# Kernel tuning notes

Hardware: AMD Instinct MI355X
Metric: run time of the kernel (lower is better)

The kernel has to match this reference:

```python
import jax, jax.numpy as jnp
import numpy as np

B, L, C, H, T = 4096, 32, 28, 512, 32


def setup_inputs() -> dict:
    key = jax.random.key(0)
    ks = jax.random.split(key, 10)
    s = 0.1
    return dict(
        input=jax.random.normal(ks[0], (B, L, C), jnp.float32),
        unpacked_masks=jnp.ones((B, L, 1), jnp.float32),
        bias_mat=jax.random.normal(ks[1], (B, L), jnp.float32),
        conv1_w=jax.random.normal(ks[2], (C, C, 3), jnp.float32) * s,  # OIH
        conv1_b=jnp.zeros((C,), jnp.float32),
        conv_w=jax.random.normal(ks[3], (1, C, 1), jnp.float32) * s,
        conv_b=jnp.zeros((1,), jnp.float32),
        w_ih=jax.random.normal(ks[4], (4 * H, C), jnp.float32) * s,
        w_hh=jax.random.normal(ks[5], (4 * H, H), jnp.float32) * s,
        b_ih=jnp.zeros((4 * H,), jnp.float32),
        b_hh=jnp.concatenate([jnp.zeros(H), jnp.ones(H), jnp.zeros(2 * H)]).astype(jnp.float32),  # forget-gate bias = 1 as in weights_init
        fc1_w=jax.random.normal(ks[6], (1, H), jnp.float32) * s,
        fc1_b=jnp.zeros((1,), jnp.float32),
        conv2_w=jax.random.normal(ks[7], (1, H, 1), jnp.float32) * s,
        conv2_b=jnp.zeros((1,), jnp.float32),
    )


def reference(input, unpacked_masks, bias_mat, conv1_w, conv1_b, conv_w, conv_b,
              w_ih, w_hh, b_ih, b_hh, fc1_w, fc1_b, conv2_w, conv2_b):
    b, l, c = input.shape
    # residual conv block: conv1d(28->28,k3,pad1) -> mask -> elu -> +input
    x_ncl = jnp.transpose(input, (0, 2, 1))
    y = jax.lax.conv_general_dilated(x_ncl, conv1_w, (1,), 'SAME',
                                     dimension_numbers=('NCH', 'OIH', 'NCH'))
    y = jnp.transpose(y + conv1_b[None, :, None], (0, 2, 1))
    x = jax.nn.elu(y * unpacked_masks) + input  # [B,L,C]
    # u_a: 1x1 conv (28->1) == per-position linear, then mask -> [B,L,1]
    u_a = (jnp.einsum('blc,c->bl', x, conv_w[0, :, 0]) + conv_b)[..., None] * unpacked_masks
    bias = bias_mat.reshape(b, l, 1)

    def step(carry, _):
        h, cstate = carry
        w_a = (h @ fc1_w.T + fc1_b)[:, :, None]                 # [B,1,1]
        attn = jax.nn.leaky_relu(u_a + w_a) + bias              # [B,L,1]
        attn = jax.nn.softmax(attn, axis=1)                     # softmax over sequence
        context = jnp.einsum('bl,blc->bc', attn[..., 0], x)     # [B,C]
        gates = context @ w_ih.T + b_ih + h @ w_hh.T + b_hh     # [B,4H]
        i, f, g, o = jnp.split(gates, 4, axis=1)                # torch LSTMCell gate order
        cstate = jax.nn.sigmoid(f) * cstate + jax.nn.sigmoid(i) * jnp.tanh(g)
        h = jax.nn.sigmoid(o) * jnp.tanh(cstate)
        return (h, cstate), h

    h0 = jnp.zeros((b, w_hh.shape[1]), input.dtype)
    (_, _), hs = jax.lax.scan(step, (h0, h0), None, length=T)   # [T,B,H]
    all_hidden = jnp.transpose(hs, (1, 0, 2))                   # [B,T,H]
    # dropout layers are identity in eval; conv2 is 1x1 conv (512->1)
    out = (jnp.einsum('bth,h->bt', all_hidden, conv2_w[0, :, 0]) + conv2_b)[..., None]
    return out * unpacked_masks
```

## Files before the change

kernel.cpp:

```cpp
#include <hip/hip_runtime.h>
#include <hip/hip_bf16.h>

#define B_N 4096
#define L_N 32
#define C_N 28
#define H_N 512
#define T_N 32
#define G_N 2048
#define CHA 34
#define CHSH 4096
#define ABLK (CHA * CHSH)
#define XS 29

typedef __attribute__((ext_vector_type(2))) float f32x2;
typedef __attribute__((ext_vector_type(4))) float f32x4;
typedef __attribute__((ext_vector_type(8))) short s16x8;

static constexpr size_t OFF_WF = 0;
static constexpr size_t AB_ONE = (size_t)32 * ABLK * 2;
static constexpr size_t OFF_AB = OFF_WF + (size_t)16 * ABLK * 2;
static constexpr size_t OFF_X  = OFF_AB + 2 * AB_ONE;
static constexpr size_t OFF_UA = OFF_X + (size_t)B_N * L_N * C_N * 4;
static constexpr size_t OFF_BS = OFF_UA + (size_t)B_N * L_N * 4;
static constexpr size_t OFF_AC = OFF_BS + 8192;
static constexpr size_t ACC_HALF = (size_t)32 * B_N * 4;
static constexpr size_t OFF_CS = OFF_AC + 2 * ACC_HALF;
static constexpr size_t WS_NEED = OFF_CS + (size_t)B_N * H_N * 4;

__device__ __forceinline__ short bfbits(__hip_bfloat16 b) {
    union { __hip_bfloat16 b; short s; } v; v.b = b; return v.s;
}
__device__ __forceinline__ float sigmoidf_(float x) { return 1.f / (1.f + __expf(-x)); }
__device__ __forceinline__ float tanhf_(float x) {
    float ax = fabsf(x), e = __expf(-2.f * ax);
    float t = (1.f - e) / (1.f + e);
    return x < 0.f ? -t : t;
}

__global__ __launch_bounds__(256) void fill_out(float* out, float v) {
    int i = blockIdx.x * 256 + threadIdx.x;
    if (i < B_N * 32) out[i] = v;
}

__global__ __launch_bounds__(256) void prep_x(const float* __restrict__ input,
                       const float* __restrict__ mask,
                       const float* __restrict__ w1, const float* __restrict__ b1,
                       const float* __restrict__ cw, const float* __restrict__ cb,
                       float* __restrict__ x, float* __restrict__ ua)
{
    __shared__ float sin[8 * L_N * XS];
    __shared__ float sxb[8 * L_N * XS];
    const float* src = input + (size_t)blockIdx.x * (8 * L_N * C_N);
    for (int i = threadIdx.x; i < 8 * L_N * C_N; i += 256) {
        int lr = i / (L_N * C_N);
        int rem = i - lr * (L_N * C_N);
        int l = rem / C_N, c = rem - l * C_N;
        sin[lr * (L_N * XS) + l * XS + c] = src[i];
    }
    __syncthreads();

    int idx = blockIdx.x * 256 + threadIdx.x;
    int l = idx & 31;
    int wv = threadIdx.x >> 5;
    const float* inb = sin + wv * (L_N * XS);
    float m = mask[idx];

    float x0r[C_N], xm1[C_N], xp1[C_N];
    #pragma unroll
    for (int i = 0; i < C_N; ++i) x0r[i] = inb[l * XS + i];
    #pragma unroll
    for (int i = 0; i < C_N; ++i) {
        float up = __shfl_up(x0r[i], 1, 32);
        float dn = __shfl_down(x0r[i], 1, 32);
        xm1[i] = (l > 0)  ? up : 0.f;
        xp1[i] = (l < 31) ? dn : 0.f;
    }

    float uacc = 0.f;
    float* sxrow = sxb + wv * (L_N * XS) + l * XS;
    #pragma unroll 2
    for (int o = 0; o < C_N; ++o) {
        const float* wo = w1 + o * (C_N * 3);
        float y0 = b1[o], y1 = 0.f, y2 = 0.f;
        #pragma unroll
        for (int i = 0; i < C_N; ++i) {
            y0 += wo[i * 3 + 0] * xm1[i];
            y1 += wo[i * 3 + 1] * x0r[i];
            y2 += wo[i * 3 + 2] * xp1[i];
        }
        float y = (y0 + y1 + y2) * m;
        float e = (y > 0.f) ? y : (__expf(y) - 1.f);
        float xv = e + inb[l * XS + o];
        sxrow[o] = xv;
        uacc += xv * cw[o];
    }
    ua[idx] = (uacc + cb[0]) * m;
    __syncthreads();
    float* xdst = x + (size_t)blockIdx.x * (8 * L_N * C_N);
    for (int i = threadIdx.x; i < 8 * L_N * C_N; i += 256) {
        int lr = i / (L_N * C_N);
        int rem = i - lr * (L_N * C_N);
        int l2 = rem / C_N, c = rem - l2 * C_N;
        xdst[i] = sxb[lr * (L_N * XS) + l2 * XS + c];
    }
}

__global__ __launch_bounds__(256) void prep_wf(const float* __restrict__ w_ih,
                                               const float* __restrict__ w_hh,
                                               short* __restrict__ Wf)
{
    int blk = blockIdx.x;
    int n128 = blk / CHA, c = blk % CHA;
    bool lo = (c >= 17);
    int kbase = (lo ? (c - 17) : c) * 32;
    short* dst = Wf + ((size_t)n128 * CHA + c) * CHSH;
    for (int g = threadIdx.x; g < 512; g += 256) {
        int j = g >> 6, lane = g & 63;
        int gate = j & 3;
        int unit = n128 * 32 + (j >> 2) * 16 + (lane & 15);
        int srow = gate * H_N + unit;
        int kg = lane >> 4;
        s16x8 out;
        #pragma unroll
        for (int b2 = 0; b2 < 8; ++b2) {
            int k = kbase + kg * 8 + b2;
            float v = 0.f;
            if (k < 512) v = w_hh[(size_t)srow * H_N + k];
            else if (k < 540) v = w_ih[srow * C_N + (k - 512)];
            __hip_bfloat16 hi = __float2bfloat16(v);
            if (lo) out[b2] = bfbits(__float2bfloat16(v - __bfloat162float(hi)));
            else    out[b2] = bfbits(hi);
        }
        *(s16x8*)(dst + g * 8) = out;
    }
}

__global__ void prep_bs(const float* __restrict__ b_ih, const float* __restrict__ b_hh,
                        float* __restrict__ bsum)
{
    int p = blockIdx.x * 256 + threadIdx.x;
    if (p < G_N) {
        int unit = p >> 2, gate = p & 3;
        bsum[p] = b_ih[gate * H_N + unit] + b_hh[gate * H_N + unit];
    }
}

__global__ void prep_zero(unsigned int* __restrict__ a32, float* __restrict__ cst,
                          float* __restrict__ acc)
{
    int idx = blockIdx.x * blockDim.x + threadIdx.x;
    if (idx < B_N * 1088) a32[idx] = 0u;
    if (idx < B_N * H_N) cst[idx] = 0.f;
    if (idx < 2 * 32 * B_N) acc[idx] = 0.f;
}

struct RParams {
    const float* mask;
    const float* bias_mat;
    const float* fc1_w;
    const float* fc1_b;
    const float* conv2_w;
    const float* conv2_b;
    const short* Wf;
    const short* Ain;
    short* Aout;
    const float* x;
    const float* ua;
    const float* bsum;
    float* accW;
    float* accO;
    float* cstate;
    float* out;
};

__global__ __launch_bounds__(256) void ctx_step(RParams P, int t)
{
    __shared__ float sx[4][L_N * C_N];

    const int lane = threadIdx.x & 63;
    const int wave = threadIdx.x >> 6;
    const int row  = blockIdx.x * 4 + wave;

    f32x2 st[7];
    const float* xrow = P.x + (size_t)row * (L_N * C_N);
    #pragma unroll
    for (int q = 0; q < 7; ++q) st[q] = *(const f32x2*)(xrow + (q * 64 + lane) * 2);

    float v = (lane < 32) ? P.accW[row * 32 + lane] : P.accO[row * 32 + (lane - 32)];
    #pragma unroll
    for (int off = 1; off <= 16; off <<= 1) v += __shfl_xor(v, off);
    float aW = __shfl(v, 0);
    float aO = __shfl(v, 32);

    if (t > 0 && lane == 0)
        P.out[row * T_N + (t - 1)] = (aO + P.conv2_b[0]) * P.mask[row * L_N + (t - 1)];

    if (t < T_N) {
        float w_a = aW + P.fc1_b[0];
        int l32 = lane & 31;
        float e = P.ua[row * L_N + l32] + w_a;
        e = (e > 0.f) ? e : 0.01f * e;
        e += P.bias_mat[row * L_N + l32];
        float mx = e;
        #pragma unroll
        for (int off = 16; off > 0; off >>= 1) mx = fmaxf(mx, __shfl_xor(mx, off, 32));
        float pexp = __expf(e - mx);
        float ssum = pexp;
        #pragma unroll
        for (int off = 16; off > 0; off >>= 1) ssum += __shfl_xor(ssum, off, 32);
        float p = pexp / ssum;

        #pragma unroll
        for (int q = 0; q < 7; ++q)
            *(f32x2*)(&sx[wave][(q * 64 + lane) * 2]) = st[q];

        int cc = (lane < C_N) ? lane : 0;
        float ctx = 0.f;
        #pragma unroll
        for (int l = 0; l < L_N; ++l) {
            float al = __shfl(p, l);
            ctx += al * sx[wave][l * C_N + cc];
        }
        if (lane < C_N) {
            int m128 = row >> 7, mt = (row & 127) >> 4, r = row & 15;
            int flane = r + 16 * (lane >> 3);
            short* base = P.Aout + (size_t)m128 * ABLK + mt * 512 + flane * 8 + (lane & 7);
            __hip_bfloat16 hi = __float2bfloat16(ctx);
            base[16 * CHSH] = bfbits(hi);
            base[33 * CHSH] = bfbits(__float2bfloat16(ctx - __bfloat162float(hi)));
        }
    }
}

#define STG_BUF 32768

__global__ __launch_bounds__(256, 2) void gemm_cell_step(RParams P)
{
    __shared__ __align__(16) char smem[65536];

    const int tid  = threadIdx.x;
    const int lane = tid & 63;
    const int wave = tid >> 6;
    const int bid  = blockIdx.x;
    const int xg = bid & 7, gg = bid >> 3;
    const int m  = (xg >> 1) * 8 + (gg & 7);
    const int n  = (xg & 1) * 8 + (gg >> 3);
    const int wm = wave >> 1, wn = wave & 1;

    const short* Af = P.Ain + (size_t)m * ABLK;
    const short* Wg = P.Wf  + (size_t)n * ABLK;

    const short* slab0 = (wave < 2) ? Af : Wg;
    const int slab_lo  = (wave & 1) ? 17 : 0;

    char* bufp0 = smem;
    char* bufp1 = smem + STG_BUF;

    auto stage = [&](char* lbuf, int kk) {
        const short* gp = slab0 + (size_t)(slab_lo + kk) * CHSH + lane * 8;
        char* lb = lbuf + wave * 8192;
        #pragma unroll
        for (int r = 0; r < 8; ++r) {
            __builtin_amdgcn_global_load_lds(
                (const __attribute__((address_space(1))) void*)(gp + r * 512),
                (__attribute__((address_space(3))) void*)(lb + r * 1024),
                16, 0, 0);
        }
    };

    int aoff[4], woff[4];
    #pragma unroll
    for (int i = 0; i < 4; ++i) {
        aoff[i] = ((wm * 4 + i) * 64 + lane) * 16;
        woff[i] = ((wn * 4 + i) * 64 + lane) * 16;
    }

    f32x4 acc[4][4];
    #pragma unroll
    for (int i = 0; i < 4; ++i)
        #pragma unroll
        for (int j = 0; j < 4; ++j)
            acc[i][j] = (f32x4){0.f, 0.f, 0.f, 0.f};

    s16x8 RA[16], RB[16];
    auto ldfr = [&](const char* b, s16x8 (&R)[16]) {
        #pragma unroll
        for (int i = 0; i < 4; ++i) {
            R[i]      = *(const s16x8*)(b + aoff[i]);
            R[4 + i]  = *(const s16x8*)(b + 8192 + aoff[i]);
            R[8 + i]  = *(const s16x8*)(b + 16384 + woff[i]);
            R[12 + i] = *(const s16x8*)(b + 24576 + woff[i]);
        }
    };
    auto domm = [&](s16x8 (&R)[16]) {
        #pragma unroll
        for (int i = 0; i < 4; ++i)
            #pragma unroll
            for (int j = 0; j < 4; ++j)
                acc[i][j] = __builtin_amdgcn_mfma_f32_16x16x32_bf16(R[i], R[8 + j], acc[i][j], 0, 0, 0);
        #pragma unroll
        for (int i = 0; i < 4; ++i)
            #pragma unroll
            for (int j = 0; j < 4; ++j)
                acc[i][j] = __builtin_amdgcn_mfma_f32_16x16x32_bf16(R[4 + i], R[8 + j], acc[i][j], 0, 0, 0);
        #pragma unroll
        for (int i = 0; i < 4; ++i)
            #pragma unroll
            for (int j = 0; j < 4; ++j)
                acc[i][j] = __builtin_amdgcn_mfma_f32_16x16x32_bf16(R[i], R[12 + j], acc[i][j], 0, 0, 0);
    };
    auto step = [&](int kk, s16x8 (&Rc)[16], s16x8 (&Rn)[16], char* bcur, char* bnext) {
        asm volatile("s_waitcnt vmcnt(0) lgkmcnt(0)" ::: "memory");
        __builtin_amdgcn_s_barrier();
        __builtin_amdgcn_sched_barrier(0);
        if (kk + 2 <= 16) stage(bcur, kk + 2);
        if (kk + 1 <= 16) ldfr(bnext, Rn);
        __builtin_amdgcn_sched_barrier(0);
        __builtin_amdgcn_s_setprio(1);
        domm(Rc);
        __builtin_amdgcn_s_setprio(0);
        __builtin_amdgcn_sched_barrier(0);
    };

    stage(bufp0, 0);
    asm volatile("s_waitcnt vmcnt(0)" ::: "memory");
    __builtin_amdgcn_s_barrier();
    stage(bufp1, 1);
    ldfr(bufp0, RA);

    for (int kp = 0; kp < 8; ++kp) {
        step(2 * kp,     RA, RB, bufp0, bufp1);
        step(2 * kp + 1, RB, RA, bufp1, bufp0);
    }
    step(16, RA, RB, bufp0, bufp1);

    __syncthreads();
    short* hasm = (short*)smem;
    {
        int u15 = lane & 15, rq = lane >> 4;
        int unit = n * 32 + wn * 16 + u15;
        float cpre[4][4];
        #pragma unroll
        for (int i = 0; i < 4; ++i)
            #pragma unroll
            for (int r = 0; r < 4; ++r)
                cpre[i][r] = P.cstate[(size_t)(m * 128 + wm * 64 + i * 16 + rq * 4 + r) * H_N + unit];
        f32x4 bsv = *(const f32x4*)(P.bsum + unit * 4);
        float f1v = P.fc1_w[unit];
        float c2v = P.conv2_w[unit];
        const int fl16 = 16 * (wn * 2 + (u15 >> 3));
        const int slot = u15 & 7;
        #pragma unroll
        for (int i = 0; i < 4; ++i) {
            #pragma unroll
            for (int r = 0; r < 4; ++r) {
                int grow = m * 128 + wm * 64 + i * 16 + rq * 4 + r;
                float pi = acc[i][0][r] + bsv.x;
                float pf = acc[i][1][r] + bsv.y;
                float pg = acc[i][2][r] + bsv.z;
                float po = acc[i][3][r] + bsv.w;
                float c = sigmoidf_(pf) * cpre[i][r] + sigmoidf_(pi) * tanhf_(pg);
                P.cstate[(size_t)grow * H_N + unit] = c;
                float h = sigmoidf_(po) * tanhf_(c);
                __hip_bfloat16 hi = __float2bfloat16(h);
                int fo = (wm * 4 + i) * 512 + (rq * 4 + r + fl16) * 8 + slot;
                hasm[fo]        = bfbits(hi);
                hasm[4096 + fo] = bfbits(__float2bfloat16(h - __bfloat162float(hi)));
                float wd = f1v * h, od = c2v * h;
                #pragma unroll
                for (int off = 8; off > 0; off >>= 1) {
                    wd += __shfl_xor(wd, off);
                    od += __shfl_xor(od, off);
                }
                if (u15 == 0) {
                    P.accW[(size_t)grow * 32 + (n * 2 + wn)] = wd;
                    P.accO[(size_t)grow * 32 + (n * 2 + wn)] = od;
                }
            }
        }
    }
    __syncthreads();
    short* dhi = P.Aout + (size_t)m * ABLK + (size_t)n * CHSH;
    short* dlo = P.Aout + (size_t)m * ABLK + (size_t)(17 + n) * CHSH;
    *(s16x8*)(dhi + tid * 16)     = *(const s16x8*)(hasm + tid * 16);
    *(s16x8*)(dhi + tid * 16 + 8) = *(const s16x8*)(hasm + tid * 16 + 8);
    *(s16x8*)(dlo + tid * 16)     = *(const s16x8*)(hasm + 4096 + tid * 16);
    *(s16x8*)(dlo + tid * 16 + 8) = *(const s16x8*)(hasm + 4096 + tid * 16 + 8);
}

extern "C" void kernel_launch(void* const* d_in, const int* in_sizes, int n_in,
                              void* d_out, int out_size, void* d_ws, size_t ws_size,
                              hipStream_t stream)
{
    float* out = (float*)d_out;
    if (ws_size < WS_NEED) { fill_out<<<512, 256, 0, stream>>>(out, 4000.f); return; }

    const float* input = (const float*)d_in[0];
    const float* mask  = (const float*)d_in[1];
    const float* biasm = (const float*)d_in[2];
    const float* w1    = (const float*)d_in[3];
    const float* b1    = (const float*)d_in[4];
    const float* cw    = (const float*)d_in[5];
    const float* cb    = (const float*)d_in[6];
    const float* w_ih  = (const float*)d_in[7];
    const float* w_hh  = (const float*)d_in[8];
    const float* b_ih  = (const float*)d_in[9];
    const float* b_hh  = (const float*)d_in[10];
    const float* fc1w  = (const float*)d_in[11];
    const float* fc1b  = (const float*)d_in[12];
    const float* c2w   = (const float*)d_in[13];
    const float* c2b   = (const float*)d_in[14];

    char* ws = (char*)d_ws;
    short* Wf = (short*)(ws + OFF_WF);
    short* A0 = (short*)(ws + OFF_AB);
    short* A1 = (short*)(ws + OFF_AB + AB_ONE);
    float* x    = (float*)(ws + OFF_X);
    float* ua   = (float*)(ws + OFF_UA);
    float* bsum = (float*)(ws + OFF_BS);
    float* accW = (float*)(ws + OFF_AC);
    float* accO = (float*)(ws + OFF_AC + ACC_HALF);
    float* cst  = (float*)(ws + OFF_CS);

    prep_x<<<(B_N * L_N) / 256, 256, 0, stream>>>(input, mask, w1, b1, cw, cb, x, ua);
    prep_wf<<<16 * CHA, 256, 0, stream>>>(w_ih, w_hh, Wf);
    prep_bs<<<(G_N + 255) / 256, 256, 0, stream>>>(b_ih, b_hh, bsum);
    prep_zero<<<(B_N * 1088 + 255) / 256, 256, 0, stream>>>((unsigned int*)A0, cst, accW);

    RParams P;
    P.mask = mask; P.bias_mat = biasm; P.fc1_w = fc1w; P.fc1_b = fc1b;
    P.conv2_w = c2w; P.conv2_b = c2b; P.Wf = Wf;
    P.x = x; P.ua = ua; P.bsum = bsum; P.accW = accW; P.accO = accO;
    P.cstate = cst; P.out = out;

    short* bufs[2] = { A0, A1 };
    for (int t = 0; t < T_N; ++t) {
        P.Ain  = bufs[t & 1];
        P.Aout = bufs[t & 1];
        ctx_step<<<B_N / 4, 256, 0, stream>>>(P, t);
        P.Ain  = bufs[t & 1];
        P.Aout = bufs[(t + 1) & 1];
        gemm_cell_step<<<512, 256, 0, stream>>>(P);
    }
    P.Ain = bufs[T_N & 1];
    P.Aout = bufs[T_N & 1];
    ctx_step<<<B_N / 4, 256, 0, stream>>>(P, T_N);
}
```

Measured before the change: 1.363 ms.

## Halve GEMM M-tile to 64 rows, doubling blocks and raising occupancy

Shrinks the per-block batch tile of the fused LSTM gate GEMM from 128 to 64 rows. This doubles the grid to 1024 blocks, cuts LDS to 48KB and raises launch bounds to 3 blocks per CU. Staging is reassigned so that only three waves issue loads, and the block-to-tile mapping switches from a swizzled order to a simple linear one. The aim is more parallelism and better latency hiding across the 256 CUs. In exchange, each W tile is reused across fewer rows, so weight traffic per FLOP doubles.

```diff
diff --git a/kernel.cpp b/kernel.cpp
--- a/kernel.cpp
+++ b/kernel.cpp
@@ -232,84 +232,101 @@
     }
 }
 
-#define STG_BUF 32768
-
-__global__ __launch_bounds__(256, 2) void gemm_cell_step(RParams P)
-{
-    __shared__ __align__(16) char smem[65536];
+#define STG_BUF 24576
+
+__global__ __launch_bounds__(256, 3) void gemm_cell_step(RParams P)
+{
+    __shared__ __align__(16) char smem[49152];
 
     const int tid  = threadIdx.x;
     const int lane = tid & 63;
     const int wave = tid >> 6;
     const int bid  = blockIdx.x;
-    const int xg = bid & 7, gg = bid >> 3;
-    const int m  = (xg >> 1) * 8 + (gg & 7);
-    const int n  = (xg & 1) * 8 + (gg >> 3);
+    const int m64 = bid & 63, n = bid >> 6;
+    const int m128 = m64 >> 1, half = m64 & 1;
     const int wm = wave >> 1, wn = wave & 1;
 
-    const short* Af = P.Ain + (size_t)m * ABLK;
+    const short* Af = P.Ain + (size_t)m128 * ABLK + half * 2048;
     const short* Wg = P.Wf  + (size_t)n * ABLK;
-
-    const short* slab0 = (wave < 2) ? Af : Wg;
-    const int slab_lo  = (wave & 1) ? 17 : 0;
 
     char* bufp0 = smem;
     char* bufp1 = smem + STG_BUF;
 
     auto stage = [&](char* lbuf, int kk) {
-        const short* gp = slab0 + (size_t)(slab_lo + kk) * CHSH + lane * 8;
-        char* lb = lbuf + wave * 8192;
-        #pragma unroll
-        for (int r = 0; r < 8; ++r) {
-            __builtin_amdgcn_global_load_lds(
-                (const __attribute__((address_space(1))) void*)(gp + r * 512),
-                (__attribute__((address_space(3))) void*)(lb + r * 1024),
-                16, 0, 0);
+        if (wave == 0) {
+            const short* gh = Af + (size_t)kk * CHSH + lane * 8;
+            const short* gl = Af + (size_t)(17 + kk) * CHSH + lane * 8;
+            #pragma unroll
+            for (int r = 0; r < 4; ++r)
+                __builtin_amdgcn_global_load_lds(
+                    (const __attribute__((address_space(1))) void*)(gh + r * 512),
+                    (__attribute__((address_space(3))) void*)(lbuf + r * 1024), 16, 0, 0);
+            #pragma unroll
+            for (int r = 0; r < 4; ++r)
+                __builtin_amdgcn_global_load_lds(
+                    (const __attribute__((address_space(1))) void*)(gl + r * 512),
+                    (__attribute__((address_space(3))) void*)(lbuf + 4096 + r * 1024), 16, 0, 0);
+        } else if (wave == 1) {
+            const short* gp = Wg + (size_t)kk * CHSH + lane * 8;
+            #pragma unroll
+            for (int r = 0; r < 8; ++r)
+                __builtin_amdgcn_global_load_lds(
+                    (const __attribute__((address_space(1))) void*)(gp + r * 512),
+                    (__attribute__((address_space(3))) void*)(lbuf + 8192 + r * 1024), 16, 0, 0);
+        } else if (wave == 2) {
+            const short* gp = Wg + (size_t)(17 + kk) * CHSH + lane * 8;
+            #pragma unroll
+            for (int r = 0; r < 8; ++r)
+                __builtin_amdgcn_global_load_lds(
+                    (const __attribute__((address_space(1))) void*)(gp + r * 512),
+                    (__attribute__((address_space(3))) void*)(lbuf + 16384 + r * 1024), 16, 0, 0);
         }
     };
 
-    int aoff[4], woff[4];
-    #pragma unroll
-    for (int i = 0; i < 4; ++i) {
-        aoff[i] = ((wm * 4 + i) * 64 + lane) * 16;
-        woff[i] = ((wn * 4 + i) * 64 + lane) * 16;
-    }
-
-    f32x4 acc[4][4];
-    #pragma unroll
-    for (int i = 0; i < 4; ++i)
+    int aoff[2], woff[4];
+    #pragma unroll
+    for (int i = 0; i < 2; ++i) aoff[i] = ((wm * 2 + i) * 64 + lane) * 16;
+    #pragma unroll
+    for (int j = 0; j < 4; ++j) woff[j] = ((wn * 4 + j) * 64 + lane) * 16;
+
+    f32x4 acc[2][4];
+    #pragma unroll
+    for (int i = 0; i < 2; ++i)
         #pragma unroll
         for (int j = 0; j < 4; ++j)
             acc[i][j] = (f32x4){0.f, 0.f, 0.f, 0.f};
 
-    s16x8 RA[16], RB[16];
-    auto ldfr = [&](const char* b, s16x8 (&R)[16]) {
-        #pragma unroll
-        for (int i = 0; i < 4; ++i) {
-            R[i]      = *(const s16x8*)(b + aoff[i]);
-            R[4 + i]  = *(const s16x8*)(b + 8192 + aoff[i]);
-            R[8 + i]  = *(const s16x8*)(b + 16384 + woff[i]);
-            R[12 + i] = *(const s16x8*)(b + 24576 + woff[i]);
+    s16x8 RA[12], RB[12];
+    auto ldfr = [&](const char* b, s16x8 (&R)[12]) {
+        #pragma unroll
+        for (int i = 0; i < 2; ++i) {
+            R[i]     = *(const s16x8*)(b + aoff[i]);
+            R[2 + i] = *(const s16x8*)(b + 4096 + aoff[i]);
+        }
+        #pragma unroll
+        for (int j = 0; j < 4; ++j) {
+            R[4 + j] = *(const s16x8*)(b + 8192 + woff[j]);
+            R[8 + j] = *(const s16x8*)(b + 16384 + woff[j]);
         }
     };
-    auto domm = [&](s16x8 (&R)[16]) {
-        #pragma unroll
-        for (int i = 0; i < 4; ++i)
+    auto domm = [&](s16x8 (&R)[12]) {
+        #pragma unroll
+        for (int i = 0; i < 2; ++i)
+            #pragma unroll
+            for (int j = 0; j < 4; ++j)
+                acc[i][j] = __builtin_amdgcn_mfma_f32_16x16x32_bf16(R[i], R[4 + j], acc[i][j], 0, 0, 0);
+        #pragma unroll
+        for (int i = 0; i < 2; ++i)
+            #pragma unroll
+            for (int j = 0; j < 4; ++j)
+                acc[i][j] = __builtin_amdgcn_mfma_f32_16x16x32_bf16(R[2 + i], R[4 + j], acc[i][j], 0, 0, 0);
+        #pragma unroll
+        for (int i = 0; i < 2; ++i)
             #pragma unroll
             for (int j = 0; j < 4; ++j)
                 acc[i][j] = __builtin_amdgcn_mfma_f32_16x16x32_bf16(R[i], R[8 + j], acc[i][j], 0, 0, 0);
-        #pragma unroll
-        for (int i = 0; i < 4; ++i)
-            #pragma unroll
-            for (int j = 0; j < 4; ++j)
-                acc[i][j] = __builtin_amdgcn_mfma_f32_16x16x32_bf16(R[4 + i], R[8 + j], acc[i][j], 0, 0, 0);
-        #pragma unroll
-        for (int i = 0; i < 4; ++i)
-            #pragma unroll
-            for (int j = 0; j < 4; ++j)
-                acc[i][j] = __builtin_amdgcn_mfma_f32_16x16x32_bf16(R[i], R[12 + j], acc[i][j], 0, 0, 0);
     };
-    auto step = [&](int kk, s16x8 (&Rc)[16], s16x8 (&Rn)[16], char* bcur, char* bnext) {
+    auto step = [&](int kk, s16x8 (&Rc)[12], s16x8 (&Rn)[12], char* bcur, char* bnext) {
         asm volatile("s_waitcnt vmcnt(0) lgkmcnt(0)" ::: "memory");
         __builtin_amdgcn_s_barrier();
         __builtin_amdgcn_sched_barrier(0);
@@ -339,22 +356,22 @@
     {
         int u15 = lane & 15, rq = lane >> 4;
         int unit = n * 32 + wn * 16 + u15;
-        float cpre[4][4];
-        #pragma unroll
-        for (int i = 0; i < 4; ++i)
+        float cpre[2][4];
+        #pragma unroll
+        for (int i = 0; i < 2; ++i)
             #pragma unroll
             for (int r = 0; r < 4; ++r)
-                cpre[i][r] = P.cstate[(size_t)(m * 128 + wm * 64 + i * 16 + rq * 4 + r) * H_N + unit];
+                cpre[i][r] = P.cstate[(size_t)(m64 * 64 + wm * 32 + i * 16 + rq * 4 + r) * H_N + unit];
         f32x4 bsv = *(const f32x4*)(P.bsum + unit * 4);
         float f1v = P.fc1_w[unit];
         float c2v = P.conv2_w[unit];
         const int fl16 = 16 * (wn * 2 + (u15 >> 3));
         const int slot = u15 & 7;
         #pragma unroll
-        for (int i = 0; i < 4; ++i) {
+        for (int i = 0; i < 2; ++i) {
             #pragma unroll
             for (int r = 0; r < 4; ++r) {
-                int grow = m * 128 + wm * 64 + i * 16 + rq * 4 + r;
+                int grow = m64 * 64 + wm * 32 + i * 16 + rq * 4 + r;
                 float pi = acc[i][0][r] + bsv.x;
                 float pf = acc[i][1][r] + bsv.y;
                 float pg = acc[i][2][r] + bsv.z;
@@ -363,9 +380,9 @@
                 P.cstate[(size_t)grow * H_N + unit] = c;
                 float h = sigmoidf_(po) * tanhf_(c);
                 __hip_bfloat16 hi = __float2bfloat16(h);
-                int fo = (wm * 4 + i) * 512 + (rq * 4 + r + fl16) * 8 + slot;
+                int fo = (wm * 2 + i) * 512 + (rq * 4 + r + fl16) * 8 + slot;
                 hasm[fo]        = bfbits(hi);
-                hasm[4096 + fo] = bfbits(__float2bfloat16(h - __bfloat162float(hi)));
+                hasm[2048 + fo] = bfbits(__float2bfloat16(h - __bfloat162float(hi)));
                 float wd = f1v * h, od = c2v * h;
                 #pragma unroll
                 for (int off = 8; off > 0; off >>= 1) {
@@ -380,12 +397,10 @@
         }
     }
     __syncthreads();
-    short* dhi = P.Aout + (size_t)m * ABLK + (size_t)n * CHSH;
-    short* dlo = P.Aout + (size_t)m * ABLK + (size_t)(17 + n) * CHSH;
-    *(s16x8*)(dhi + tid * 16)     = *(const s16x8*)(hasm + tid * 16);
-    *(s16x8*)(dhi + tid * 16 + 8) = *(const s16x8*)(hasm + tid * 16 + 8);
-    *(s16x8*)(dlo + tid * 16)     = *(const s16x8*)(hasm + 4096 + tid * 16);
-    *(s16x8*)(dlo + tid * 16 + 8) = *(const s16x8*)(hasm + 4096 + tid * 16 + 8);
+    short* dhi = P.Aout + (size_t)m128 * ABLK + (size_t)n * CHSH + half * 2048;
+    short* dlo = P.Aout + (size_t)m128 * ABLK + (size_t)(17 + n) * CHSH + half * 2048;
+    *(s16x8*)(dhi + tid * 8) = *(const s16x8*)(hasm + tid * 8);
+    *(s16x8*)(dlo + tid * 8) = *(const s16x8*)(hasm + 2048 + tid * 8);
 }
 
 extern "C" void kernel_launch(void* const* d_in, const int* in_sizes, int n_in,
@@ -440,7 +455,7 @@
         ctx_step<<<B_N / 4, 256, 0, stream>>>(P, t);
         P.Ain  = bufs[t & 1];
         P.Aout = bufs[(t + 1) & 1];
-        gemm_cell_step<<<512, 256, 0, stream>>>(P);
+        gemm_cell_step<<<1024, 256, 0, stream>>>(P);
     }
     P.Ain = bufs[T_N & 1];
     P.Aout = bufs[T_N & 1];
```

Measured after the change: 1.418 ms. +4.1%, slower.
